# Performance work log

Measured on AMD Instinct MI355X. Metric: run time of the kernel, lower is better.

The kernel has to match this reference:

```python
import jax, jax.numpy as jnp
import numpy as np

N, E, NFEAT, NHID, H = 25000, 400000, 256, 32, 12
NEG_SLOPE = 0.2


def setup_inputs() -> dict:
    key = jax.random.key(0)
    ks = jax.random.split(key, 16)
    g = lambda k, shp, s=0.05: jax.random.normal(k, shp, dtype=jnp.float32) * s
    return {
        "x": jax.random.normal(ks[0], (N, NFEAT), dtype=jnp.float32),
        "edge_index": jax.random.randint(ks[1], (2, E), 0, N, dtype=jnp.int64),
        "edge_attr": jax.random.normal(ks[2], (E, NHID), dtype=jnp.float32),
        # conv1: in=NFEAT -> H heads x NHID, edge_dim=NHID, concat=True
        "W1": g(ks[3], (NFEAT, H * NHID)),
        "att_src1": g(ks[4], (H, NHID)),
        "att_dst1": g(ks[5], (H, NHID)),
        "W_e1": g(ks[6], (NHID, H * NHID)),
        "att_edge1": g(ks[7], (H, NHID)),
        "b1": jnp.zeros((H * NHID,), jnp.float32),
        # conv2: in=H*NHID -> H heads x NHID, concat=False (mean over heads)
        "W2": g(ks[8], (H * NHID, H * NHID)),
        "att_src2": g(ks[9], (H, NHID)),
        "att_dst2": g(ks[10], (H, NHID)),
        "b2": jnp.zeros((NHID,), jnp.float32),
    }


def gat_layer(x, edge_index, W, att_src, att_dst, bias, concat,
              edge_attr=None, W_e=None, att_e=None):
    n = x.shape[0]
    h, c = att_src.shape
    hx = (x @ W).reshape(n, h, c)                      # [N,H,C]
    a_s = jnp.sum(hx * att_src, axis=-1)               # [N,H]
    a_d = jnp.sum(hx * att_dst, axis=-1)               # [N,H]
    src, dst = edge_index[0], edge_index[1]
    loop = jnp.arange(n)
    if edge_attr is not None:
        # PyG add_self_loops fill_value='mean': mean of incoming edge_attr per dst
        cnt = jax.ops.segment_sum(jnp.ones(dst.shape[0], jnp.float32), dst, n)
        loop_attr = jax.ops.segment_sum(edge_attr, dst, n) / jnp.maximum(cnt, 1.0)[:, None]
        edge_attr = jnp.concatenate([edge_attr, loop_attr], axis=0)
    src = jnp.concatenate([src, loop])
    dst = jnp.concatenate([dst, loop])
    e = a_s[src] + a_d[dst]                            # [E+N,H]
    if edge_attr is not None:
        he = (edge_attr @ W_e).reshape(-1, h, c)
        e = e + jnp.sum(he * att_e, axis=-1)
    e = jax.nn.leaky_relu(e, NEG_SLOPE)
    # segment softmax over destination nodes (every node has a self loop -> no empty segments)
    m = jax.ops.segment_max(e, dst, n)                 # [N,H]
    ex = jnp.exp(e - m[dst])
    den = jax.ops.segment_sum(ex, dst, n)
    alpha = ex / den[dst]                              # [E+N,H]
    out = jax.ops.segment_sum(alpha[:, :, None] * hx[src], dst, n)  # [N,H,C]
    out = out.reshape(n, h * c) if concat else out.mean(axis=1)
    return out + bias


def reference(x, edge_index, edge_attr, W1, att_src1, att_dst1, W_e1, att_edge1, b1,
              W2, att_src2, att_dst2, b2):
    # eval mode: all F.dropout / GATConv dropout are identity
    h1 = gat_layer(x, edge_index, W1, att_src1, att_dst1, b1, True,
                   edge_attr, W_e1, att_edge1)
    h1 = jax.nn.elu(h1)
    h2 = gat_layer(h1, edge_index, W2, att_src2, att_dst2, b2, False)
    return h2, jax.nn.log_softmax(h2, axis=1)
```

## Files before the change

### kernel.cpp

```cpp
#include <hip/hip_runtime.h>
#include <hip/hip_bf16.h>
#include <math.h>

#define N_NODES 25000
#define N_EDGES 400000
#define NFEAT   256
#define NHID    32
#define NHEAD   12
#define HC      384
#define NEG_SLOPE 0.2f
#define NBLK    ((N_NODES + 255) / 256)
#define BPAD    40

typedef __attribute__((ext_vector_type(8))) short short8;
typedef __attribute__((ext_vector_type(4))) float floatx4;

__device__ __forceinline__ float bf2f(unsigned short u) {
    union { unsigned int i; float f; } v; v.i = ((unsigned int)u) << 16; return v.f;
}
__device__ __forceinline__ unsigned short f2bf(float f) {
    union { float f; unsigned int i; } v; v.f = f;
    unsigned int x = v.i;
    unsigned int r = (x + 0x7FFFu + ((x >> 16) & 1u)) >> 16;
    return (unsigned short)r;
}
__device__ __forceinline__ int clampN(int s) {
    return ((unsigned)s < (unsigned)N_NODES) ? s : 0;
}
__device__ __forceinline__ float ldf(const void* p, size_t i, int isF32) {
    return isF32 ? ((const float*)p)[i] : bf2f(((const unsigned short*)p)[i]);
}
__device__ __forceinline__ int ldi(const void* p, size_t i, int isI64) {
    return isI64 ? (int)((const unsigned int*)p)[2 * i] : ((const int*)p)[i];
}

__device__ __forceinline__ void fma8(float* acc, float a, uint4 g) {
    unsigned int u[4] = {g.x, g.y, g.z, g.w};
#pragma unroll
    for (int i = 0; i < 4; i++) {
        union { unsigned int i; float f; } lo, hi;
        lo.i = u[i] << 16;
        hi.i = u[i] & 0xFFFF0000u;
        acc[2 * i]     += a * lo.f;
        acc[2 * i + 1] += a * hi.f;
    }
}
__device__ __forceinline__ void mul8(float* acc, float a, uint4 g) {
    unsigned int u[4] = {g.x, g.y, g.z, g.w};
#pragma unroll
    for (int i = 0; i < 4; i++) {
        union { unsigned int i; float f; } lo, hi;
        lo.i = u[i] << 16;
        hi.i = u[i] & 0xFFFF0000u;
        acc[2 * i]     = a * lo.f;
        acc[2 * i + 1] = a * hi.f;
    }
}

__global__ void detect_kernel(const unsigned short* __restrict__ xr,
                              const unsigned int* __restrict__ eir,
                              int* __restrict__ flags) {
    __shared__ int sF, sI;
    if (threadIdx.x == 0) { sF = 0; sI = 0; }
    __syncthreads();
    int t = threadIdx.x;
    int cf = 0, ci = 0;
#pragma unroll
    for (int i = 0; i < 4; i++) {
        unsigned short u = xr[2 * (t * 4 + i)];
        int e = (u >> 7) & 0xFF;
        if (e >= 100 && e <= 140) cf++;
        unsigned int v = eir[2 * (t * 4 + i) + 1];
        if (v == 0u) ci++;
    }
    atomicAdd(&sF, cf);
    atomicAdd(&sI, ci);
    __syncthreads();
    if (threadIdx.x == 0) {
        flags[0] = (sF >= 614) ? 0 : 1;
        flags[1] = (sI >= 512) ? 1 : 0;
    }
}

__global__ void prep_kernel(const void* __restrict__ We1,
                            const void* __restrict__ att_e,
                            const void* __restrict__ W1,
                            const void* __restrict__ W2,
                            const int* __restrict__ flags,
                            float* __restrict__ M1,
                            unsigned short* __restrict__ Wt1,
                            unsigned short* __restrict__ Wt2) {
    int isF32 = flags[0];
    int id = blockIdx.x * 256 + threadIdx.x;
    if (id < 384) {
        int k = id / 12, h = id % 12;
        float s = 0.f;
        for (int c = 0; c < 32; c++)
            s += ldf(We1, (size_t)k * HC + h * 32 + c, isF32) *
                 ldf(att_e, (size_t)h * 32 + c, isF32);
        M1[k * 12 + h] = s;
        return;
    }
    int id1 = id - 384;
    if (id1 < 384 * 256) {
        int n = id1 / 256, k = id1 % 256;
        Wt1[(size_t)n * 256 + k] = f2bf(ldf(W1, (size_t)k * HC + n, isF32));
        return;
    }
    int id2 = id1 - 384 * 256;
    if (id2 < 384 * 384) {
        int n = id2 / 384, k = id2 % 384;
        Wt2[(size_t)n * 384 + k] = f2bf(ldf(W2, (size_t)k * HC + n, isF32));
    }
}

__global__ void hist_kernel(const void* __restrict__ ei, const int* __restrict__ flags,
                            int* __restrict__ cnt) {
    int isI64 = flags[1];
    int e = blockIdx.x * 256 + threadIdx.x;
    if (e < N_EDGES) {
        int d = clampN(ldi(ei, (size_t)N_EDGES + e, isI64));
        atomicAdd(&cnt[d], 1);
    }
}

__global__ void blockscan_kernel(const int* __restrict__ cnt, int* __restrict__ incl,
                                 int* __restrict__ bsum) {
    __shared__ int buf[256];
    int i = blockIdx.x * 256 + threadIdx.x;
    int v = (i < N_NODES) ? cnt[i] : 0;
    buf[threadIdx.x] = v;
    __syncthreads();
    for (int off = 1; off < 256; off <<= 1) {
        int t = (threadIdx.x >= off) ? buf[threadIdx.x - off] : 0;
        __syncthreads();
        buf[threadIdx.x] += t;
        __syncthreads();
    }
    if (i < N_NODES) incl[i] = buf[threadIdx.x];
    if (threadIdx.x == 255) bsum[blockIdx.x] = buf[255];
}

__global__ void bscan_kernel(const int* __restrict__ bsum, int* __restrict__ boff) {
    __shared__ int buf[128];
    int t = threadIdx.x;
    int v = (t < NBLK) ? bsum[t] : 0;
    buf[t] = v;
    __syncthreads();
    for (int off = 1; off < 128; off <<= 1) {
        int u = (t >= off) ? buf[t - off] : 0;
        __syncthreads();
        buf[t] += u;
        __syncthreads();
    }
    if (t < NBLK) boff[t] = buf[t] - v;
}

__global__ void finalize_kernel(const int* __restrict__ incl, const int* __restrict__ boff,
                                const int* __restrict__ cnt,
                                int* __restrict__ rowptr, int* __restrict__ wofs) {
    int i = blockIdx.x * 256 + threadIdx.x;
    if (i == 0) rowptr[0] = 0;
    if (i < N_NODES) {
        int v = incl[i] + boff[blockIdx.x];
        rowptr[i + 1] = v;
        wofs[i] = v - cnt[i];
    }
}

__global__ void scatter_kernel(const void* __restrict__ ei, const int* __restrict__ flags,
                               int* __restrict__ wofs, int2* __restrict__ pairs) {
    int isI64 = flags[1];
    int e = blockIdx.x * 256 + threadIdx.x;
    if (e >= N_EDGES) return;
    int d = clampN(ldi(ei, (size_t)N_EDGES + e, isI64));
    int pos = atomicAdd(&wofs[d], 1);
    if ((unsigned)pos >= (unsigned)N_EDGES) return;
    pairs[pos] = make_int2(clampN(ldi(ei, (size_t)e, isI64)), e);
}

__global__ void ae_kernel(const void* __restrict__ ea, const int* __restrict__ flags,
                          const float* __restrict__ M1,
                          unsigned short* __restrict__ ae_edge) {
    __shared__ float sM[384];
    for (int i = threadIdx.x; i < 384; i += 256) sM[i] = M1[i];
    __syncthreads();
    int isF32 = flags[0];
    int e = blockIdx.x * 256 + threadIdx.x;
    if (e >= N_EDGES) return;
    float a[32];
    if (isF32) {
        const float4* r4 = (const float4*)((const float*)ea + (size_t)e * 32);
#pragma unroll
        for (int i = 0; i < 8; i++) {
            float4 v = r4[i];
            a[4 * i] = v.x; a[4 * i + 1] = v.y; a[4 * i + 2] = v.z; a[4 * i + 3] = v.w;
        }
    } else {
        const unsigned short* r = (const unsigned short*)ea + (size_t)e * 32;
#pragma unroll
        for (int i = 0; i < 32; i++) a[i] = bf2f(r[i]);
    }
    float ev[12];
#pragma unroll
    for (int h = 0; h < 12; h++) ev[h] = 0.f;
#pragma unroll
    for (int k = 0; k < 32; k++)
#pragma unroll
        for (int h = 0; h < 12; h++) ev[h] += a[k] * sM[k * 12 + h];
    unsigned int w[6];
#pragma unroll
    for (int i = 0; i < 6; i++)
        w[i] = (unsigned int)f2bf(ev[2 * i]) | ((unsigned int)f2bf(ev[2 * i + 1]) << 16);
    uint2* dst = (uint2*)(ae_edge + (size_t)e * 12);
    dst[0] = make_uint2(w[0], w[1]);
    dst[1] = make_uint2(w[2], w[3]);
    dst[2] = make_uint2(w[4], w[5]);
}

__global__ __launch_bounds__(512) void gemm_mfma(const void* __restrict__ A,
                                                 const unsigned short* __restrict__ Bt,
                                                 const int* __restrict__ flags,
                                                 int aFromFlag,
                                                 unsigned short* __restrict__ C,
                                                 int M, int K) {
    __shared__ unsigned short sB[384 * BPAD];
    int aF32 = aFromFlag ? flags[0] : 0;
    int lane = threadIdx.x & 63;
    int w = threadIdx.x >> 6;
    int m0 = blockIdx.x * 64 + (w >> 1) * 16;
    int c0 = (w & 1) * 192;
    int r = lane & 15, q = lane >> 4;
    int row = m0 + r;
    if (row >= M) row = M - 1;
    floatx4 acc[12];
#pragma unroll
    for (int j = 0; j < 12; j++) acc[j] = (floatx4){0.f, 0.f, 0.f, 0.f};
    for (int k0 = 0; k0 < K; k0 += 32) {
        for (int i = threadIdx.x; i < 384 * 4; i += 512) {
            int col = i >> 2, seg = i & 3;
            *(uint4*)(sB + (size_t)col * BPAD + seg * 8) =
                *(const uint4*)(Bt + (size_t)col * K + k0 + seg * 8);
        }
        __syncthreads();
        short8 a;
        if (aF32) {
            const float4* ap = (const float4*)((const float*)A + (size_t)row * K + k0 + q * 8);
            float4 u = ap[0], v = ap[1];
            a[0] = (short)f2bf(u.x); a[1] = (short)f2bf(u.y);
            a[2] = (short)f2bf(u.z); a[3] = (short)f2bf(u.w);
            a[4] = (short)f2bf(v.x); a[5] = (short)f2bf(v.y);
            a[6] = (short)f2bf(v.z); a[7] = (short)f2bf(v.w);
        } else {
            a = *(const short8*)((const unsigned short*)A + (size_t)row * K + k0 + q * 8);
        }
#pragma unroll
        for (int j = 0; j < 12; j++) {
            int col = c0 + 16 * j + r;
            short8 b = *(const short8*)(sB + (size_t)col * BPAD + q * 8);
            acc[j] = __builtin_amdgcn_mfma_f32_16x16x32_bf16(a, b, acc[j], 0, 0, 0);
        }
        __syncthreads();
    }
#pragma unroll
    for (int j = 0; j < 12; j++) {
        int col = c0 + 16 * j + r;
#pragma unroll
        for (int t = 0; t < 4; t++) {
            int orow = m0 + q * 4 + t;
            if (orow < M) C[(size_t)orow * HC + col] = f2bf(acc[j][t]);
        }
    }
}

__global__ __launch_bounds__(256) void att_kernel(const unsigned short* __restrict__ hx,
                           const void* __restrict__ att_src,
                           const void* __restrict__ att_dst,
                           const int* __restrict__ flags,
                           float* __restrict__ a_s, float* __restrict__ a_d) {
    __shared__ float sS[12 * 33];
    __shared__ float sD[12 * 33];
    int isF32 = flags[0];
    for (int i = threadIdx.x; i < 384; i += 256) {
        int hh = i >> 5, c = i & 31;
        sS[hh * 33 + c] = ldf(att_src, (size_t)i, isF32);
        sD[hh * 33 + c] = ldf(att_dst, (size_t)i, isF32);
    }
    __syncthreads();
    int id = blockIdx.x * 256 + threadIdx.x;
    if (id >= N_NODES * NHEAD) return;
    int n = id / NHEAD;
    int h = id - n * NHEAD;
    const short8* row = (const short8*)(hx + (size_t)n * HC + h * 32);
    float s = 0.f, d = 0.f;
#pragma unroll
    for (int i = 0; i < 4; i++) {
        short8 v = row[i];
#pragma unroll
        for (int j = 0; j < 8; j++) {
            float f = bf2f((unsigned short)v[j]);
            int c = i * 8 + j;
            s += f * sS[h * 33 + c];
            d += f * sD[h * 33 + c];
        }
    }
    a_s[id] = s;
    a_d[id] = d;
}

__global__ __launch_bounds__(256) void softmax_kernel(const float* __restrict__ a_s,
                                                      const float* __restrict__ a_d,
                                                      const int* __restrict__ rowptr,
                                                      const int2* __restrict__ pairs,
                                                      const unsigned short* __restrict__ ae_edge,
                                                      unsigned short* __restrict__ alpha_e,
                                                      float* __restrict__ exl_out,
                                                      float* __restrict__ rden_out,
                                                      int has_ae) {
    int id = blockIdx.x * 256 + threadIdx.x;
    if (id >= N_NODES * NHEAD) return;
    int node = id / NHEAD;
    int h = id - node * NHEAD;
    int start = rowptr[node], end = rowptr[node + 1];
    if (start < 0) start = 0;
    if (end > N_EDGES) end = N_EDGES;
    int deg = end - start;
    float adn = a_d[id];
    float asn = a_s[id];
    float mx = -1e30f, sae = 0.f;
    for (int p = start; p < end; p += 2) {
        int2 pe0 = pairs[p];
        bool two = (p + 1 < end);
        int2 pe1 = two ? pairs[p + 1] : pe0;
        int s0 = clampN(pe0.x), s1 = clampN(pe1.x);
        float v0 = a_s[(size_t)s0 * NHEAD + h] + adn;
        float v1 = a_s[(size_t)s1 * NHEAD + h] + adn;
        if (has_ae) {
            int e0 = ((unsigned)pe0.y < (unsigned)N_EDGES) ? pe0.y : 0;
            int e1 = ((unsigned)pe1.y < (unsigned)N_EDGES) ? pe1.y : 0;
            float a0 = bf2f(ae_edge[(size_t)e0 * NHEAD + h]);
            float a1 = bf2f(ae_edge[(size_t)e1 * NHEAD + h]);
            v0 += a0; sae += a0;
            if (two) { v1 += a1; sae += a1; }
        }
        v0 = v0 > 0.f ? v0 : NEG_SLOPE * v0;
        v1 = v1 > 0.f ? v1 : NEG_SLOPE * v1;
        mx = fmaxf(mx, v0);
        if (two) mx = fmaxf(mx, v1);
    }
    float invdeg = 1.f / fmaxf((float)deg, 1.f);
    float el = asn + adn + (has_ae ? sae * invdeg : 0.f);
    el = el > 0.f ? el : NEG_SLOPE * el;
    mx = fmaxf(mx, el);
    float den = 0.f;
    for (int p = start; p < end; p += 2) {
        int2 pe0 = pairs[p];
        bool two = (p + 1 < end);
        int2 pe1 = two ? pairs[p + 1] : pe0;
        int s0 = clampN(pe0.x), s1 = clampN(pe1.x);
        float v0 = a_s[(size_t)s0 * NHEAD + h] + adn;
        float v1 = a_s[(size_t)s1 * NHEAD + h] + adn;
        if (has_ae) {
            int e0 = ((unsigned)pe0.y < (unsigned)N_EDGES) ? pe0.y : 0;
            int e1 = ((unsigned)pe1.y < (unsigned)N_EDGES) ? pe1.y : 0;
            v0 += bf2f(ae_edge[(size_t)e0 * NHEAD + h]);
            v1 += bf2f(ae_edge[(size_t)e1 * NHEAD + h]);
        }
        v0 = v0 > 0.f ? v0 : NEG_SLOPE * v0;
        v1 = v1 > 0.f ? v1 : NEG_SLOPE * v1;
        float ex0 = expf(v0 - mx);
        float ex1 = expf(v1 - mx);
        alpha_e[(size_t)p * NHEAD + h] = f2bf(ex0);
        den += ex0;
        if (two) {
            alpha_e[(size_t)(p + 1) * NHEAD + h] = f2bf(ex1);
            den += ex1;
        }
    }
    float exl = expf(el - mx);
    exl_out[id] = exl;
    rden_out[id] = 1.f / (den + exl);
}

__global__ __launch_bounds__(256) void agg1_kernel(const unsigned short* __restrict__ hx,
                                                   const unsigned short* __restrict__ alpha_e,
                                                   const float* __restrict__ exl,
                                                   const float* __restrict__ rden,
                                                   const int* __restrict__ rowptr,
                                                   const int2* __restrict__ pairs,
                                                   const void* __restrict__ b1,
                                                   const int* __restrict__ flags,
                                                   unsigned short* __restrict__ h1) {
    int isF32 = flags[0];
    int lane = threadIdx.x & 63;
    int node = blockIdx.x * 4 + (threadIdx.x >> 6);
    if (node >= N_NODES || lane >= 48) return;
    int h = lane >> 2;
    int off = lane * 8;
    int start = rowptr[node], end = rowptr[node + 1];
    if (start < 0) start = 0;
    if (end > N_EDGES) end = N_EDGES;
    float acc[8];
    {
        uint4 g = *(const uint4*)(hx + (size_t)node * HC + off);
        mul8(acc, exl[node * 12 + h], g);
    }
    int p = start;
    int2 pe0, pe1, pe2, pe3;
    bool have = (p + 4 <= end);
    if (have) {
        pe0 = pairs[p]; pe1 = pairs[p + 1]; pe2 = pairs[p + 2]; pe3 = pairs[p + 3];
    }
    while (have) {
        int2 c0 = pe0, c1 = pe1, c2 = pe2, c3 = pe3;
        bool nxt = (p + 8 <= end);
        if (nxt) {
            pe0 = pairs[p + 4]; pe1 = pairs[p + 5]; pe2 = pairs[p + 6]; pe3 = pairs[p + 7];
        }
        uint4 g0 = *(const uint4*)(hx + (size_t)clampN(c0.x) * HC + off);
        uint4 g1 = *(const uint4*)(hx + (size_t)clampN(c1.x) * HC + off);
        uint4 g2 = *(const uint4*)(hx + (size_t)clampN(c2.x) * HC + off);
        uint4 g3 = *(const uint4*)(hx + (size_t)clampN(c3.x) * HC + off);
        float a0 = bf2f(alpha_e[(size_t)p * 12 + h]);
        float a1 = bf2f(alpha_e[(size_t)(p + 1) * 12 + h]);
        float a2 = bf2f(alpha_e[(size_t)(p + 2) * 12 + h]);
        float a3 = bf2f(alpha_e[(size_t)(p + 3) * 12 + h]);
        fma8(acc, a0, g0);
        fma8(acc, a1, g1);
        fma8(acc, a2, g2);
        fma8(acc, a3, g3);
        p += 4;
        have = nxt;
    }
    for (; p < end; p++) {
        int2 pe = pairs[p];
        uint4 g = *(const uint4*)(hx + (size_t)clampN(pe.x) * HC + off);
        float a = bf2f(alpha_e[(size_t)p * 12 + h]);
        fma8(acc, a, g);
    }
    float rd = rden[node * 12 + h];
    unsigned int w[4];
#pragma unroll
    for (int i = 0; i < 4; i++) {
        float v0 = acc[2 * i] * rd + ldf(b1, (size_t)(off + 2 * i), isF32);
        float v1 = acc[2 * i + 1] * rd + ldf(b1, (size_t)(off + 2 * i + 1), isF32);
        v0 = v0 > 0.f ? v0 : expm1f(v0);
        v1 = v1 > 0.f ? v1 : expm1f(v1);
        w[i] = (unsigned int)f2bf(v0) | ((unsigned int)f2bf(v1) << 16);
    }
    *(uint4*)(h1 + (size_t)node * HC + off) = make_uint4(w[0], w[1], w[2], w[3]);
}

__global__ __launch_bounds__(256) void agg2_kernel(const unsigned short* __restrict__ hx,
                                                   const unsigned short* __restrict__ alpha_e,
                                                   const float* __restrict__ exl,
                                                   const float* __restrict__ rden,
                                                   const int* __restrict__ rowptr,
                                                   const int2* __restrict__ pairs,
                                                   const void* __restrict__ b2,
                                                   const int* __restrict__ flags,
                                                   float* __restrict__ out) {
    int isF32 = flags[0];
    int lane = threadIdx.x & 63;
    int node = blockIdx.x * 4 + (threadIdx.x >> 6);
    if (node >= N_NODES) return;
    bool act = lane < 48;
    int h = act ? (lane >> 2) : 0;
    int off = act ? lane * 8 : 0;
    float acc[8];
#pragma unroll
    for (int k = 0; k < 8; k++) acc[k] = 0.f;
    if (act) {
        int start = rowptr[node], end = rowptr[node + 1];
        if (start < 0) start = 0;
        if (end > N_EDGES) end = N_EDGES;
        {
            uint4 g = *(const uint4*)(hx + (size_t)node * HC + off);
            mul8(acc, exl[node * 12 + h], g);
        }
        int p = start;
        int2 pe0, pe1, pe2, pe3;
        bool have = (p + 4 <= end);
        if (have) {
            pe0 = pairs[p]; pe1 = pairs[p + 1]; pe2 = pairs[p + 2]; pe3 = pairs[p + 3];
        }
        while (have) {
            int2 c0 = pe0, c1 = pe1, c2 = pe2, c3 = pe3;
            bool nxt = (p + 8 <= end);
            if (nxt) {
                pe0 = pairs[p + 4]; pe1 = pairs[p + 5]; pe2 = pairs[p + 6]; pe3 = pairs[p + 7];
            }
            uint4 g0 = *(const uint4*)(hx + (size_t)clampN(c0.x) * HC + off);
            uint4 g1 = *(const uint4*)(hx + (size_t)clampN(c1.x) * HC + off);
            uint4 g2 = *(const uint4*)(hx + (size_t)clampN(c2.x) * HC + off);
            uint4 g3 = *(const uint4*)(hx + (size_t)clampN(c3.x) * HC + off);
            float a0 = bf2f(alpha_e[(size_t)p * 12 + h]);
            float a1 = bf2f(alpha_e[(size_t)(p + 1) * 12 + h]);
            float a2 = bf2f(alpha_e[(size_t)(p + 2) * 12 + h]);
            float a3 = bf2f(alpha_e[(size_t)(p + 3) * 12 + h]);
            fma8(acc, a0, g0);
            fma8(acc, a1, g1);
            fma8(acc, a2, g2);
            fma8(acc, a3, g3);
            p += 4;
            have = nxt;
        }
        for (; p < end; p++) {
            int2 pe = pairs[p];
            uint4 g = *(const uint4*)(hx + (size_t)clampN(pe.x) * HC + off);
            float a = bf2f(alpha_e[(size_t)p * 12 + h]);
            fma8(acc, a, g);
        }
        float rd = rden[node * 12 + h];
#pragma unroll
        for (int k = 0; k < 8; k++) acc[k] *= rd;
    }
#pragma unroll
    for (int k = 0; k < 8; k++) {
        float t1 = __shfl(acc[k], lane + 16);
        float t2 = __shfl(acc[k], lane + 32);
        acc[k] += t1 + t2;
        acc[k] += __shfl_xor(acc[k], 4);
        acc[k] += __shfl_xor(acc[k], 8);
    }
    if (lane < 4) {
        int q = lane;
        float hv[8];
        float m = -1e30f;
#pragma unroll
        for (int t = 0; t < 8; t++) {
            hv[t] = acc[t] * (1.f / 12.f) + ldf(b2, (size_t)(8 * q + t), isF32);
            m = fmaxf(m, hv[t]);
        }
        m = fmaxf(m, __shfl_xor(m, 1));
        m = fmaxf(m, __shfl_xor(m, 2));
        float s = 0.f;
#pragma unroll
        for (int t = 0; t < 8; t++) s += expf(hv[t] - m);
        s += __shfl_xor(s, 1);
        s += __shfl_xor(s, 2);
        float ls = m + logf(s);
        float4* o0 = (float4*)(out + (size_t)node * 32 + 8 * q);
        float4* l0 = (float4*)(out + (size_t)N_NODES * 32 + (size_t)node * 32 + 8 * q);
        o0[0] = make_float4(hv[0], hv[1], hv[2], hv[3]);
        o0[1] = make_float4(hv[4], hv[5], hv[6], hv[7]);
        l0[0] = make_float4(hv[0] - ls, hv[1] - ls, hv[2] - ls, hv[3] - ls);
        l0[1] = make_float4(hv[4] - ls, hv[5] - ls, hv[6] - ls, hv[7] - ls);
    }
}

extern "C" void kernel_launch(void* const* d_in, const int* in_sizes, int n_in,
                              void* d_out, int out_size, void* d_ws, size_t ws_size,
                              hipStream_t stream) {
    const void* x        = d_in[0];
    const void* ei       = d_in[1];
    const void* ea       = d_in[2];
    const void* W1       = d_in[3];
    const void* att_src1 = d_in[4];
    const void* att_dst1 = d_in[5];
    const void* We1      = d_in[6];
    const void* att_e1   = d_in[7];
    const void* b1       = d_in[8];
    const void* W2       = d_in[9];
    const void* att_src2 = d_in[10];
    const void* att_dst2 = d_in[11];
    const void* b2       = d_in[12];
    float* out = (float*)d_out;

    char* ws = (char*)d_ws;
    size_t off = 0;
    auto alloc = [&](size_t bytes) -> void* {
        void* p = ws + off;
        off = (off + bytes + 255) & ~(size_t)255;
        return p;
    };
    int*            flags   = (int*)alloc(16);
    float*          M1      = (float*)alloc((size_t)384 * 4);
    int*            rowptr  = (int*)alloc((size_t)(N_NODES + 1) * 4);
    int*            cnt     = (int*)alloc((size_t)N_NODES * 4);
    int*            wofs    = (int*)alloc((size_t)N_NODES * 4);
    int*            incl    = (int*)alloc((size_t)N_NODES * 4);
    int*            bsum    = (int*)alloc((size_t)NBLK * 4);
    int*            boff    = (int*)alloc((size_t)NBLK * 4);
    float*          a_s     = (float*)alloc((size_t)N_NODES * 12 * 4);
    float*          a_d     = (float*)alloc((size_t)N_NODES * 12 * 4);
    float*          exl     = (float*)alloc((size_t)N_NODES * 12 * 4);
    float*          rden    = (float*)alloc((size_t)N_NODES * 12 * 4);
    int2*           pairs   = (int2*)alloc((size_t)N_EDGES * 8);
    unsigned short* alpha_e = (unsigned short*)alloc((size_t)N_EDGES * 12 * 2);
    unsigned short* hx      = (unsigned short*)alloc((size_t)N_NODES * HC * 2);
    unsigned short* h1      = (unsigned short*)alloc((size_t)N_NODES * HC * 2);
    unsigned short* ae_edge = h1;
    unsigned short* Wt1     = (unsigned short*)alloc((size_t)384 * 256 * 2);
    unsigned short* Wt2     = (unsigned short*)alloc((size_t)384 * 384 * 2);

    hipMemsetAsync(cnt, 0, (size_t)N_NODES * 4, stream);
    detect_kernel<<<1, 256, 0, stream>>>((const unsigned short*)x, (const unsigned int*)ei, flags);
    prep_kernel<<<(384 + 384 * 256 + 384 * 384 + 255) / 256, 256, 0, stream>>>(
        We1, att_e1, W1, W2, flags, M1, Wt1, Wt2);
    hist_kernel<<<(N_EDGES + 255) / 256, 256, 0, stream>>>(ei, flags, cnt);
    blockscan_kernel<<<NBLK, 256, 0, stream>>>(cnt, incl, bsum);
    bscan_kernel<<<1, 128, 0, stream>>>(bsum, boff);
    finalize_kernel<<<NBLK, 256, 0, stream>>>(incl, boff, cnt, rowptr, wofs);
    scatter_kernel<<<(N_EDGES + 255) / 256, 256, 0, stream>>>(ei, flags, wofs, pairs);
    ae_kernel<<<(N_EDGES + 255) / 256, 256, 0, stream>>>(ea, flags, M1, ae_edge);
    gemm_mfma<<<(N_NODES + 63) / 64, 512, 0, stream>>>(x, Wt1, flags, 1, hx, N_NODES, NFEAT);
    att_kernel<<<(N_NODES * 12 + 255) / 256, 256, 0, stream>>>(hx, att_src1, att_dst1, flags,
                                                               a_s, a_d);
    softmax_kernel<<<(N_NODES * 12 + 255) / 256, 256, 0, stream>>>(a_s, a_d, rowptr, pairs,
                                                                   ae_edge, alpha_e, exl, rden, 1);
    agg1_kernel<<<(N_NODES + 3) / 4, 256, 0, stream>>>(hx, alpha_e, exl, rden, rowptr, pairs,
                                                       b1, flags, h1);
    gemm_mfma<<<(N_NODES + 63) / 64, 512, 0, stream>>>(h1, Wt2, flags, 0, hx, N_NODES, HC);
    att_kernel<<<(N_NODES * 12 + 255) / 256, 256, 0, stream>>>(hx, att_src2, att_dst2, flags,
                                                               a_s, a_d);
    softmax_kernel<<<(N_NODES * 12 + 255) / 256, 256, 0, stream>>>(a_s, a_d, rowptr, pairs,
                                                                   ae_edge, alpha_e, exl, rden, 0);
    agg2_kernel<<<(N_NODES + 3) / 4, 256, 0, stream>>>(hx, alpha_e, exl, rden, rowptr, pairs,
                                                       b2, flags, out);
}
```

Measured before the change: 421.6 us.

## Split layer-1 aggregation across channel groups with 42 nodes per block

```diff
diff --git a/kernel.cpp b/kernel.cpp
--- a/kernel.cpp
+++ b/kernel.cpp
@@ -11,6 +11,7 @@
 #define NEG_SLOPE 0.2f
 #define NBLK    ((N_NODES + 255) / 256)
 #define BPAD    40
+#define NPB     42
 
 typedef __attribute__((ext_vector_type(8))) short short8;
 typedef __attribute__((ext_vector_type(4))) float floatx4;
@@ -392,11 +393,17 @@
                                                    const int* __restrict__ flags,
                                                    unsigned short* __restrict__ h1) {
     int isF32 = flags[0];
-    int lane = threadIdx.x & 63;
-    int node = blockIdx.x * 4 + (threadIdx.x >> 6);
-    if (node >= N_NODES || lane >= 48) return;
-    int h = lane >> 2;
-    int off = lane * 8;
+    int t = threadIdx.x;
+    if (t >= NPB * 6) return;
+    int gq = blockIdx.x & 7;
+    int nb = blockIdx.x >> 3;
+    int nl = t / 6;
+    int node = nb * NPB + nl;
+    if (node >= N_NODES) return;
+    int cs = t - nl * 6;
+    int cidx = 6 * gq + cs;
+    int off = cidx * 8;
+    int h = cidx >> 2;
     int start = rowptr[node], end = rowptr[node + 1];
     if (start < 0) start = 0;
     if (end > N_EDGES) end = N_EDGES;
@@ -406,37 +413,20 @@
         mul8(acc, exl[node * 12 + h], g);
     }
     int p = start;
-    int2 pe0, pe1, pe2, pe3;
-    bool have = (p + 4 <= end);
-    if (have) {
-        pe0 = pairs[p]; pe1 = pairs[p + 1]; pe2 = pairs[p + 2]; pe3 = pairs[p + 3];
-    }
-    while (have) {
-        int2 c0 = pe0, c1 = pe1, c2 = pe2, c3 = pe3;
-        bool nxt = (p + 8 <= end);
-        if (nxt) {
-            pe0 = pairs[p + 4]; pe1 = pairs[p + 5]; pe2 = pairs[p + 6]; pe3 = pairs[p + 7];
-        }
-        uint4 g0 = *(const uint4*)(hx + (size_t)clampN(c0.x) * HC + off);
-        uint4 g1 = *(const uint4*)(hx + (size_t)clampN(c1.x) * HC + off);
-        uint4 g2 = *(const uint4*)(hx + (size_t)clampN(c2.x) * HC + off);
-        uint4 g3 = *(const uint4*)(hx + (size_t)clampN(c3.x) * HC + off);
+    for (; p + 2 <= end; p += 2) {
+        int2 pe0 = pairs[p];
+        int2 pe1 = pairs[p + 1];
+        uint4 g0 = *(const uint4*)(hx + (size_t)clampN(pe0.x) * HC + off);
+        uint4 g1 = *(const uint4*)(hx + (size_t)clampN(pe1.x) * HC + off);
         float a0 = bf2f(alpha_e[(size_t)p * 12 + h]);
         float a1 = bf2f(alpha_e[(size_t)(p + 1) * 12 + h]);
-        float a2 = bf2f(alpha_e[(size_t)(p + 2) * 12 + h]);
-        float a3 = bf2f(alpha_e[(size_t)(p + 3) * 12 + h]);
         fma8(acc, a0, g0);
         fma8(acc, a1, g1);
-        fma8(acc, a2, g2);
-        fma8(acc, a3, g3);
-        p += 4;
-        have = nxt;
-    }
-    for (; p < end; p++) {
+    }
+    if (p < end) {
         int2 pe = pairs[p];
         uint4 g = *(const uint4*)(hx + (size_t)clampN(pe.x) * HC + off);
-        float a = bf2f(alpha_e[(size_t)p * 12 + h]);
-        fma8(acc, a, g);
+        fma8(acc, bf2f(alpha_e[(size_t)p * 12 + h]), g);
     }
     float rd = rden[node * 12 + h];
     unsigned int w[4];
@@ -609,8 +599,8 @@
                                                                a_s, a_d);
     softmax_kernel<<<(N_NODES * 12 + 255) / 256, 256, 0, stream>>>(a_s, a_d, rowptr, pairs,
                                                                    ae_edge, alpha_e, exl, rden, 1);
-    agg1_kernel<<<(N_NODES + 3) / 4, 256, 0, stream>>>(hx, alpha_e, exl, rden, rowptr, pairs,
-                                                       b1, flags, h1);
+    agg1_kernel<<<((N_NODES + NPB - 1) / NPB) * 8, 256, 0, stream>>>(hx, alpha_e, exl, rden,
+                                                                     rowptr, pairs, b1, flags, h1);
     gemm_mfma<<<(N_NODES + 63) / 64, 512, 0, stream>>>(h1, Wt2, flags, 0, hx, N_NODES, HC);
     att_kernel<<<(N_NODES * 12 + 255) / 256, 256, 0, stream>>>(hx, att_src2, att_dst2, flags,
                                                                a_s, a_d);
```

Measured after the change: 471.5 us. 11.8% more time.
